# Optimization experiments

Hardware: AMD Instinct MI355X
Metric: run time of the kernel (lower is better)

Reference implementation:

```python
import jax, jax.numpy as jnp
import numpy as np

IN_CHANNELS = 512
NUM_HEADS = 8
PARTIAL = 4
PC = IN_CHANNELS // PARTIAL  # 128, per-branch dim


def _mha(x, wqkv, bqkv, wproj, bproj, num_heads):
    # Standard ViT-style attention block: fused qkv -> SDPA -> out proj.
    B, N, C = x.shape
    d = C // num_heads
    qkv = (x @ wqkv + bqkv).reshape(B, N, 3, num_heads, d)
    q, k, v = jnp.moveaxis(qkv, 2, 0)            # each (B, N, h, d)
    q = q.transpose(0, 2, 1, 3)                  # (B, h, N, d)
    k = k.transpose(0, 2, 1, 3)
    v = v.transpose(0, 2, 1, 3)
    scale = jnp.asarray(d, x.dtype) ** -0.5
    attn = jax.nn.softmax(jnp.einsum('bhqd,bhkd->bhqk', q, k) * scale, axis=-1)
    out = jnp.einsum('bhqk,bhkd->bhqd', attn, v)
    out = out.transpose(0, 2, 1, 3).reshape(B, N, C)
    return out @ wproj + bproj


def _channel_shuffle(x, groups):
    # ShuffleNet channel shuffle on (b, c, n, t)
    b, c, n, t = x.shape
    return x.reshape(b, groups, c // groups, n, t).transpose(0, 2, 1, 3, 4).reshape(b, c, n, t)


def setup_inputs() -> dict:
    key = jax.random.key(0)
    ks = jax.random.split(key, 13)
    b, n, t = 8, 25, 64
    inp = {'x': jax.random.normal(ks[0], (b, n, t, IN_CHANNELS), dtype=jnp.float32)}
    i = 1
    for name in ('t', 's', 'st'):
        inp[f'{name}_wqkv'] = jax.random.normal(ks[i], (PC, 3 * PC), dtype=jnp.float32) * 0.02; i += 1
        inp[f'{name}_bqkv'] = jnp.zeros((3 * PC,), dtype=jnp.float32)
        inp[f'{name}_wproj'] = jax.random.normal(ks[i], (PC, PC), dtype=jnp.float32) * 0.02; i += 1
        inp[f'{name}_bproj'] = jnp.zeros((PC,), dtype=jnp.float32)
    return inp


def reference(x, t_wqkv, t_bqkv, t_wproj, t_bproj,
              s_wqkv, s_bqkv, s_wproj, s_bproj,
              st_wqkv, st_bqkv, st_wproj, st_bproj):
    b, n, t, c = x.shape
    pc = PC
    # split order in forward: x_id, x_st, x_s, x_t (all width pc here)
    x_id = x[..., 0 * pc:1 * pc]
    x_st = x[..., 1 * pc:2 * pc]
    x_s = x[..., 2 * pc:3 * pc]
    x_t = x[..., 3 * pc:4 * pc]

    t_x = x_t.reshape(b * n, t, pc)                       # temporal: attend over t
    s_x = x_s.transpose(0, 2, 1, 3).reshape(b * t, n, pc)  # spatial: attend over n
    st_x = x_st.reshape(b, n * t, pc)                      # spatiotemporal: attend over n*t

    t_x = _mha(t_x, t_wqkv, t_bqkv, t_wproj, t_bproj, NUM_HEADS).reshape(b, n, t, pc)
    s_x = _mha(s_x, s_wqkv, s_bqkv, s_wproj, s_bproj, NUM_HEADS).reshape(b, t, n, pc).transpose(0, 2, 1, 3)
    st_x = _mha(st_x, st_wqkv, st_bqkv, st_wproj, st_bproj, NUM_HEADS).reshape(b, n, t, pc)

    # concat order: id, t, s, st (differs from split order), then to channels-first
    out = jnp.concatenate((x_id, t_x, s_x, st_x), axis=3).transpose(0, 3, 1, 2)  # (b, c, n, t)
    return _channel_shuffle(out, PARTIAL)
```

## Files before the change

### kernel.cpp

```cpp
#include <hip/hip_runtime.h>
#include <hip/hip_bf16.h>

#define BUF   1638400ull
#define QSC   0.36067376f

typedef __attribute__((ext_vector_type(4)))  float    f4;
typedef __attribute__((ext_vector_type(16))) float    f16v;
typedef __attribute__((ext_vector_type(8)))  short    s8v;
typedef __attribute__((ext_vector_type(4)))  unsigned u4v;

#if __has_builtin(__builtin_amdgcn_exp2f)
#define EXP2(x) __builtin_amdgcn_exp2f(x)
#else
#define EXP2(x) exp2f(x)
#endif
#if __has_builtin(__builtin_amdgcn_rcpf)
#define RCP(x) __builtin_amdgcn_rcpf(x)
#else
#define RCP(x) (1.0f/(x))
#endif

__device__ __forceinline__ short f2bf(float f) {
    __hip_bfloat16 h = __float2bfloat16(f);
    short s; __builtin_memcpy(&s, &h, 2); return s;
}
__device__ __forceinline__ unsigned pack2(float a, float b) {
    return (unsigned)(unsigned short)f2bf(a) | ((unsigned)(unsigned short)f2bf(b) << 16);
}
__device__ __forceinline__ float bf2f(short s) {
    return __uint_as_float((unsigned)(unsigned short)s << 16);
}
__device__ __forceinline__ unsigned tpack(float hi, float lo) {
    return __builtin_amdgcn_perm(__float_as_uint(hi), __float_as_uint(lo), 0x07060302u);
}
__device__ __forceinline__ f16v zf16() {
    f16v z;
#pragma unroll
    for (int i = 0; i < 16; i++) z[i] = 0.f;
    return z;
}

__global__ __launch_bounds__(256) void prep(
    const float* __restrict__ wq0, const float* __restrict__ wq1,
    const float* __restrict__ wq2,
    const float* __restrict__ wp0, const float* __restrict__ wp1,
    const float* __restrict__ wp2,
    short* __restrict__ wsw, short* __restrict__ onesb)
{
    const int blk = blockIdx.x, tid = threadIdx.x;
    if (blk < 96) {
        const int idx0 = blk * 2048 + tid * 8;
        const float* W; int Ncols, loc = idx0;
        if      (idx0 < 49152)  { W = wq0; Ncols = 384; }
        else if (idx0 < 98304)  { W = wq1; Ncols = 384; loc -= 49152; }
        else if (idx0 < 147456) { W = wq2; Ncols = 384; loc -= 98304; }
        else if (idx0 < 163840) { W = wp0; Ncols = 128; loc -= 147456; }
        else if (idx0 < 180224) { W = wp1; Ncols = 128; loc -= 163840; }
        else                    { W = wp2; Ncols = 128; loc -= 180224; }
        const int lane = (loc >> 3) & 63, ks = (loc >> 9) & 3, nt = loc >> 11;
        const int col = nt * 16 + (lane & 15);
        const int k0  = ks * 32 + 8 * (lane >> 4);
        s8v o;
#pragma unroll
        for (int j = 0; j < 8; j++) o[j] = f2bf(W[(k0 + j) * Ncols + col]);
        *(s8v*)(wsw + idx0) = o;
    } else {
        s8v o;
#pragma unroll
        for (int j = 0; j < 8; j++) o[j] = (short)0x3F80;
        *(s8v*)(onesb + tid * 8) = o;
    }
}

__global__ __launch_bounds__(256) void qkv_all(
    const float* __restrict__ x, const short* __restrict__ wsw,
    const float* __restrict__ bq0, const float* __restrict__ bq1,
    const float* __restrict__ bq2,
    short* __restrict__ q0, short* __restrict__ k0, short* __restrict__ vt0,
    short* __restrict__ q1, short* __restrict__ k1, short* __restrict__ vt1,
    short* __restrict__ q2, short* __restrict__ k2, short* __restrict__ vt2)
{
    const int br = blockIdx.x / 800, tile = blockIdx.x % 800;
    const int tok0 = tile * 16;
    const int wave = threadIdx.x >> 6, lane = threadIdx.x & 63;
    const int c = lane & 15, gq = lane >> 4;
    const int off = 384 - 128 * br;
    const short* wswb = wsw + br * 49152;
    const float* bias = (br == 0) ? bq0 : (br == 1) ? bq1 : bq2;

    const float* xrow = x + (size_t)(tok0 + c) * 512 + off + 8 * gq;
    s8v af[4];
#pragma unroll
    for (int ks = 0; ks < 4; ks++) {
        float4 a = *(const float4*)(xrow + ks * 32);
        float4 b = *(const float4*)(xrow + ks * 32 + 4);
        u4v t;
        t[0] = tpack(a.y, a.x); t[1] = tpack(a.w, a.z);
        t[2] = tpack(b.y, b.x); t[3] = tpack(b.w, b.z);
        af[ks] = __builtin_bit_cast(s8v, t);
    }

    const int batch0 = tok0 >> 6;
    const int b_  = tok0 / 1600;
    const int rm0 = tok0 - b_ * 1600;
    const int seq1 = rm0 >> 6;

    for (int nti = 0; nti < 6; nti++) {
        const int nt = wave * 6 + nti;
        const short* bp = wswb + ((size_t)(nt * 4) * 64 + lane) * 8;
        f4 acc = {0.f, 0.f, 0.f, 0.f};
#pragma unroll
        for (int ks = 0; ks < 4; ks++) {
            s8v bf = *(const s8v*)(bp + ks * 512);
            acc = __builtin_amdgcn_mfma_f32_16x16x32_bf16(af[ks], bf, acc, 0, 0, 0);
        }
        const float bv = bias[nt * 16 + c];
        const float v0 = acc[0]+bv, v1 = acc[1]+bv, v2 = acc[2]+bv, v3 = acc[3]+bv;
        const int which = nt >> 3, h = nt & 7;

        if (br == 0) {
            const int seq0 = (tok0 & 63) + 4 * gq;
            if (which == 2) {
                unsigned* p = (unsigned*)(vt0 + ((size_t)(batch0*8+h)*16 + c)*64 + seq0);
                p[0] = pack2(v0, v1); p[1] = pack2(v2, v3);
            } else {
                short* p = (which ? k0 : q0) + (((size_t)(batch0*8+h)*64 + seq0)*16 + c);
                p[0]=f2bf(v0); p[16]=f2bf(v1); p[32]=f2bf(v2); p[48]=f2bf(v3);
            }
        } else if (br == 1) {
            const int bt0 = b_ * 64 + (rm0 & 63) + 4 * gq;
            if (which == 2) {
                short* p = vt1 + ((size_t)(bt0*8+h)*16 + c)*32 + seq1;
                p[0]=f2bf(v0); p[4096]=f2bf(v1); p[8192]=f2bf(v2); p[12288]=f2bf(v3);
            } else {
                short* p = (which ? k1 : q1) + (((size_t)bt0*8+h)*25 + seq1)*16 + c;
                p[0]=f2bf(v0); p[3200]=f2bf(v1); p[6400]=f2bf(v2); p[9600]=f2bf(v3);
            }
        } else {
            const int seq0 = rm0 + 4 * gq;
            if (which == 2) {
                unsigned* p = (unsigned*)(vt2 + ((size_t)b_*128 + h*16 + c)*1600 + seq0);
                p[0] = pack2(v0, v1); p[1] = pack2(v2, v3);
            } else {
                short* p = (which ? k2 : q2) + (((size_t)b_*8+h)*1600 + seq0)*16 + c;
                p[0]=f2bf(v0); p[16]=f2bf(v1); p[32]=f2bf(v2); p[48]=f2bf(v3);
            }
        }
    }
}

template<int NSTEPS, bool MASK>
__device__ __forceinline__ void attn32(
    const short* __restrict__ qg, const short* __restrict__ kg,
    const short* __restrict__ vtg, const int vstride,
    const short* __restrict__ onesb,
    const int lane, const int qt0,
    short* __restrict__ obase, const int orowstride, const int nq)
{
    const int n = lane & 31, g2 = lane >> 5;

    s8v qraw = *(const s8v*)(qg + (size_t)(qt0 + n) * 16 + 8 * g2);
    u4v qu;
#pragma unroll
    for (int jp = 0; jp < 4; jp++)
        qu[jp] = tpack(bf2f(qraw[2*jp+1]) * QSC, bf2f(qraw[2*jp]) * QSC);
    const s8v qf = __builtin_bit_cast(s8v, qu);

    const int b4 = n >> 2;
    const int krow = ((b4 ^ (((b4 ^ (b4 >> 1)) & 1) * 3)) << 2) + (n & 3);
    const short* kp = kg + (size_t)krow * 16 + 8 * g2;
    const short* vp = (n < 16) ? (vtg + (size_t)n * vstride + 8 * g2)
                               : (onesb + 8 * g2);

    f16v oacc = zf16();

    for (int s = 0; s < NSTEPS; s++) {
        s8v kf  = *(const s8v*)kp;  kp += 512;
        s8v vf1 = *(const s8v*)vp;
        s8v vf2 = *(const s8v*)(vp + 16); vp += 32;

        f16v sacc = __builtin_amdgcn_mfma_f32_32x32x16_bf16(kf, qf, zf16(), 0, 0, 0);

        float p[16];
#pragma unroll
        for (int r = 0; r < 16; r++) {
            p[r] = EXP2(sacc[r]);
            if (MASK && r >= 9) { if (g2) p[r] = 0.f; }
        }
        u4v u1, u2;
        u1[0]=tpack(p[1],p[0]);   u1[1]=tpack(p[3],p[2]);
        u1[2]=tpack(p[5],p[4]);   u1[3]=tpack(p[7],p[6]);
        u2[0]=tpack(p[9],p[8]);   u2[1]=tpack(p[11],p[10]);
        u2[2]=tpack(p[13],p[12]); u2[3]=tpack(p[15],p[14]);
        s8v pf1 = __builtin_bit_cast(s8v, u1);
        s8v pf2 = __builtin_bit_cast(s8v, u2);

        oacc = __builtin_amdgcn_mfma_f32_32x32x16_bf16(pf1, vf1, oacc, 0, 0, 0);
        oacc = __builtin_amdgcn_mfma_f32_32x32x16_bf16(pf2, vf2, oacc, 0, 0, 0);
    }

#pragma unroll
    for (int r = 0; r < 16; r++) {
        float l = __shfl_xor(oacc[r], 16);
        float o = oacc[r] * RCP(l);
        const int q = qt0 + (r & 3) + 8 * (r >> 2) + 4 * g2;
        if (n < 16 && q < nq)
            obase[(size_t)q * orowstride + n] = f2bf(o);
    }
}

__global__ __launch_bounds__(256) void attn_all(
    const short* __restrict__ q0, const short* __restrict__ k0, const short* __restrict__ vt0,
    const short* __restrict__ q1, const short* __restrict__ k1, const short* __restrict__ vt1,
    const short* __restrict__ q2, const short* __restrict__ k2, const short* __restrict__ vt2,
    const short* __restrict__ onesb,
    short* __restrict__ ob0, short* __restrict__ ob1, short* __restrict__ ob2)
{
    const int wave = threadIdx.x >> 6, lane = threadIdx.x & 63;
    const int wid = blockIdx.x * 4 + wave;

    if (wid < 3200) {
        const int bh = wid / 50, qt0 = (wid % 50) * 32;
        const int batch = bh >> 3, h = bh & 7;
        attn32<50, false>(q2 + (size_t)bh * 25600, k2 + (size_t)bh * 25600,
                          vt2 + (size_t)batch * 204800 + (size_t)h * 16 * 1600, 1600,
                          onesb, lane, qt0,
                          ob2 + (size_t)batch * 204800 + h * 16, 128, 1600);
    } else if (wid < 6400) {
        const int w = wid - 3200;
        const int bh = w >> 1, qt0 = (w & 1) * 32;
        const int bn = bh >> 3, h = bh & 7;
        attn32<2, false>(q0 + (size_t)bh * 1024, k0 + (size_t)bh * 1024,
                         vt0 + (size_t)bh * 1024, 64,
                         onesb, lane, qt0,
                         ob0 + (size_t)bn * 8192 + h * 16, 128, 64);
    } else {
        const int bh = wid - 6400;
        if (bh < 4096) {
            const int bt = bh >> 3, h = bh & 7;
            const int b_ = bt >> 6, t_ = bt & 63;
            attn32<1, true>(q1 + (size_t)bh * 400, k1 + (size_t)bh * 400,
                            vt1 + (size_t)bh * 512, 32,
                            onesb, lane, 0,
                            ob1 + (size_t)b_ * 204800 + t_ * 128 + h * 16, 8192, 25);
        }
    }
}

__global__ __launch_bounds__(256) void projid(
    const short* __restrict__ ob0, const short* __restrict__ ob1,
    const short* __restrict__ ob2, const short* __restrict__ wsw,
    const float* __restrict__ bp0, const float* __restrict__ bp1,
    const float* __restrict__ bp2,
    const float* __restrict__ x, float* __restrict__ out)
{
    __shared__ unsigned short xl[64 * 130];
    const int blk = blockIdx.x, tid = threadIdx.x;

    if (blk < 2400) {
        const int br = blk / 800, t8 = blk % 800;
        const short* obb = (br == 0) ? ob0 : (br == 1) ? ob1 : ob2;
        const float* bp  = (br == 0) ? bp0 : (br == 1) ? bp1 : bp2;
        const short* wswb = wsw + 147456 + br * 16384;
        const int grp = br + 1;
        const int tok0 = t8 * 16;
        const int wave = tid >> 6, lane = tid & 63;
        const int c = lane & 15, gq = lane >> 4;

        s8v af[4];
#pragma unroll
        for (int ks = 0; ks < 4; ks++)
            af[ks] = *(const s8v*)(obb + (size_t)(tok0 + c) * 128 + ks * 32 + 8 * gq);

        const int bnn = t8 >> 2, b_ = bnn / 25, n_ = bnn % 25;
        const int t0 = (t8 & 3) * 16 + 4 * gq;

        for (int nti = 0; nti < 2; nti++) {
            const int nt = wave * 2 + nti;
            const short* bpw = wswb + ((size_t)(nt * 4) * 64 + lane) * 8;
            f4 acc = {0.f, 0.f, 0.f, 0.f};
#pragma unroll
            for (int ks = 0; ks < 4; ks++) {
                s8v bf = *(const s8v*)(bpw + ks * 512);
                acc = __builtin_amdgcn_mfma_f32_16x16x32_bf16(af[ks], bf, acc, 0, 0, 0);
            }
            const int c2 = nt * 16 + c;
            const float bv = bp[c2];
            float4 st = {acc[0]+bv, acc[1]+bv, acc[2]+bv, acc[3]+bv};
            *(float4*)(out + (size_t)b_ * 819200 + (size_t)(c2 * 4 + grp) * 1600
                           + n_ * 64 + t0) = st;
        }
    } else {
        const int bn = blk - 2400;
        const int b_ = bn / 25, n_ = bn % 25;
        for (int idx = tid; idx < 8192; idx += 256) {
            int row = idx >> 7, c2 = idx & 127;
            xl[row * 130 + c2] =
                (unsigned short)(__float_as_uint(x[(size_t)(bn * 64 + row) * 512 + c2]) >> 16);
        }
        __syncthreads();
        const int t_ = tid & 63, cg = tid >> 6;
        const size_t base = (size_t)b_ * 819200 + (size_t)n_ * 64 + t_;
#pragma unroll
        for (int i = 0; i < 32; i++) {
            int c2 = cg + 4 * i;
            out[base + (size_t)(c2 * 4 + 0) * 1600] =
                __uint_as_float((unsigned)xl[t_ * 130 + c2] << 16);
        }
    }
}

extern "C" void kernel_launch(void* const* d_in, const int* in_sizes, int n_in,
                              void* d_out, int out_size, void* d_ws, size_t ws_size,
                              hipStream_t stream)
{
    const float* x        = (const float*)d_in[0];
    const float* t_wqkv   = (const float*)d_in[1];
    const float* t_bqkv   = (const float*)d_in[2];
    const float* t_wproj  = (const float*)d_in[3];
    const float* t_bproj  = (const float*)d_in[4];
    const float* s_wqkv   = (const float*)d_in[5];
    const float* s_bqkv   = (const float*)d_in[6];
    const float* s_wproj  = (const float*)d_in[7];
    const float* s_bproj  = (const float*)d_in[8];
    const float* st_wqkv  = (const float*)d_in[9];
    const float* st_bqkv  = (const float*)d_in[10];
    const float* st_wproj = (const float*)d_in[11];
    const float* st_bproj = (const float*)d_in[12];

    short* wsw   = (short*)d_ws;
    short* onesb = wsw + 196608ull;
    short* q0  = onesb + 2048ull;
    short* k0  = q0 + BUF;
    short* vt0 = k0 + BUF;
    short* q1  = vt0 + BUF;
    short* k1  = q1 + BUF;
    short* vt1 = k1 + BUF;
    short* q2  = vt1 + 2097152ull;
    short* k2  = q2 + BUF;
    short* vt2 = k2 + BUF;
    short* ob0 = vt2 + BUF;
    short* ob1 = ob0 + BUF;
    short* ob2 = ob1 + BUF;
    float* out = (float*)d_out;

    prep<<<97, 256, 0, stream>>>(t_wqkv, s_wqkv, st_wqkv,
                                 t_wproj, s_wproj, st_wproj, wsw, onesb);
    qkv_all<<<2400, 256, 0, stream>>>(x, wsw, t_bqkv, s_bqkv, st_bqkv,
                                      q0, k0, vt0, q1, k1, vt1, q2, k2, vt2);
    attn_all<<<2624, 256, 0, stream>>>(q0, k0, vt0, q1, k1, vt1, q2, k2, vt2,
                                       onesb, ob0, ob1, ob2);
    projid<<<2600, 256, 0, stream>>>(ob0, ob1, ob2, wsw,
                                     t_bproj, s_bproj, st_bproj, x, out);
}
```

Measured before the change: 180.3 us.

## Split long spatiotemporal attention across four waves with shared-memory reduction

The n*t=1600-length attention branch previously ran as one wave per 32-query tile, looping over all 50 key tiles. Each such tile now gets its own block whose four waves each process a quarter of the key range. The partial (unnormalized) outputs and the row sums from the ones-column trick are added through LDS before normalization. This gives more parallelism and shorter serial chains for the long branch, at the cost of more blocks, LDS traffic, and a barrier. The grid grows accordingly. The approach is valid without a running max because scores are exponentiated directly, as in the code before.

Measured after the change: 174.8 us. 1.03x faster.

```diff
diff --git a/kernel.cpp b/kernel.cpp
--- a/kernel.cpp
+++ b/kernel.cpp
@@ -149,35 +149,38 @@
     }
 }
 
-template<int NSTEPS, bool MASK>
-__device__ __forceinline__ void attn32(
-    const short* __restrict__ qg, const short* __restrict__ kg,
-    const short* __restrict__ vtg, const int vstride,
-    const short* __restrict__ onesb,
-    const int lane, const int qt0,
-    short* __restrict__ obase, const int orowstride, const int nq)
+__device__ __forceinline__ s8v load_qfrag(const short* __restrict__ qg,
+                                          const int qt0, const int lane)
 {
     const int n = lane & 31, g2 = lane >> 5;
-
     s8v qraw = *(const s8v*)(qg + (size_t)(qt0 + n) * 16 + 8 * g2);
     u4v qu;
 #pragma unroll
     for (int jp = 0; jp < 4; jp++)
         qu[jp] = tpack(bf2f(qraw[2*jp+1]) * QSC, bf2f(qraw[2*jp]) * QSC);
-    const s8v qf = __builtin_bit_cast(s8v, qu);
-
+    return __builtin_bit_cast(s8v, qu);
+}
+
+template<bool MASK>
+__device__ __forceinline__ f16v attn_loop(
+    const short* __restrict__ kg, const short* __restrict__ vtg, const int vstride,
+    const short* __restrict__ onesb, const s8v qf, const int lane,
+    const int s0, const int s1)
+{
+    const int n = lane & 31, g2 = lane >> 5;
     const int b4 = n >> 2;
     const int krow = ((b4 ^ (((b4 ^ (b4 >> 1)) & 1) * 3)) << 2) + (n & 3);
-    const short* kp = kg + (size_t)krow * 16 + 8 * g2;
-    const short* vp = (n < 16) ? (vtg + (size_t)n * vstride + 8 * g2)
-                               : (onesb + 8 * g2);
+    const short* kp = kg + (size_t)(s0 * 32 + krow) * 16 + 8 * g2;
+    const short* vp;
+    int vinc;
+    if (n < 16) { vp = vtg + (size_t)n * vstride + s0 * 32 + 8 * g2; vinc = 32; }
+    else        { vp = onesb + 8 * g2; vinc = 0; }
 
     f16v oacc = zf16();
-
-    for (int s = 0; s < NSTEPS; s++) {
+    for (int s = s0; s < s1; s++) {
         s8v kf  = *(const s8v*)kp;  kp += 512;
         s8v vf1 = *(const s8v*)vp;
-        s8v vf2 = *(const s8v*)(vp + 16); vp += 32;
+        s8v vf2 = *(const s8v*)(vp + 16); vp += vinc;
 
         f16v sacc = __builtin_amdgcn_mfma_f32_32x32x16_bf16(kf, qf, zf16(), 0, 0, 0);
 
@@ -198,7 +201,14 @@
         oacc = __builtin_amdgcn_mfma_f32_32x32x16_bf16(pf1, vf1, oacc, 0, 0, 0);
         oacc = __builtin_amdgcn_mfma_f32_32x32x16_bf16(pf2, vf2, oacc, 0, 0, 0);
     }
-
+    return oacc;
+}
+
+__device__ __forceinline__ void attn_epilogue(
+    const f16v oacc, short* __restrict__ obase, const int orowstride,
+    const int qt0, const int nq, const int lane)
+{
+    const int n = lane & 31, g2 = lane >> 5;
 #pragma unroll
     for (int r = 0; r < 16; r++) {
         float l = __shfl_xor(oacc[r], 16);
@@ -216,34 +226,59 @@
     const short* __restrict__ onesb,
     short* __restrict__ ob0, short* __restrict__ ob1, short* __restrict__ ob2)
 {
+    __shared__ float red[4][64][16];
+    const int blk = blockIdx.x;
     const int wave = threadIdx.x >> 6, lane = threadIdx.x & 63;
-    const int wid = blockIdx.x * 4 + wave;
-
-    if (wid < 3200) {
-        const int bh = wid / 50, qt0 = (wid % 50) * 32;
+    const int n = lane & 31, g2 = lane >> 5;
+
+    if (blk < 3200) {
+        const int bh = blk / 50, qt0 = (blk % 50) * 32;
         const int batch = bh >> 3, h = bh & 7;
-        attn32<50, false>(q2 + (size_t)bh * 25600, k2 + (size_t)bh * 25600,
-                          vt2 + (size_t)batch * 204800 + (size_t)h * 16 * 1600, 1600,
-                          onesb, lane, qt0,
-                          ob2 + (size_t)batch * 204800 + h * 16, 128, 1600);
-    } else if (wid < 6400) {
-        const int w = wid - 3200;
-        const int bh = w >> 1, qt0 = (w & 1) * 32;
+        const s8v qf = load_qfrag(q2 + (size_t)bh * 25600, qt0, lane);
+        const int s0 = (50 * wave) >> 2, s1 = (50 * (wave + 1)) >> 2;
+        f16v part = attn_loop<false>(
+            k2 + (size_t)bh * 25600,
+            vt2 + (size_t)batch * 204800 + (size_t)h * 25600, 1600,
+            onesb, qf, lane, s0, s1);
+
+#pragma unroll
+        for (int j = 0; j < 4; j++) {
+            float4 v = {part[4*j], part[4*j+1], part[4*j+2], part[4*j+3]};
+            *(float4*)&red[wave][lane][4*j] = v;
+        }
+        __syncthreads();
+
+        short* obase = ob2 + (size_t)batch * 204800 + h * 16;
+#pragma unroll
+        for (int j = 0; j < 4; j++) {
+            const int r = 4 * wave + j;
+            float sum = red[0][lane][r] + red[1][lane][r]
+                      + red[2][lane][r] + red[3][lane][r];
+            float l = __shfl_xor(sum, 16);
+            float o = sum * RCP(l);
+            const int q = qt0 + (r & 3) + 8 * (r >> 2) + 4 * g2;
+            if (n < 16)
+                obase[(size_t)q * 128 + n] = f2bf(o);
+        }
+    } else if (blk < 4000) {
+        const int wid = (blk - 3200) * 4 + wave;
+        const int bh = wid >> 1, qt0 = (wid & 1) * 32;
         const int bn = bh >> 3, h = bh & 7;
-        attn32<2, false>(q0 + (size_t)bh * 1024, k0 + (size_t)bh * 1024,
-                         vt0 + (size_t)bh * 1024, 64,
-                         onesb, lane, qt0,
-                         ob0 + (size_t)bn * 8192 + h * 16, 128, 64);
+        const s8v qf = load_qfrag(q0 + (size_t)bh * 1024, qt0, lane);
+        f16v oacc = attn_loop<false>(k0 + (size_t)bh * 1024,
+                                     vt0 + (size_t)bh * 1024, 64,
+                                     onesb, qf, lane, 0, 2);
+        attn_epilogue(oacc, ob0 + (size_t)bn * 8192 + h * 16, 128, qt0, 64, lane);
     } else {
-        const int bh = wid - 6400;
-        if (bh < 4096) {
-            const int bt = bh >> 3, h = bh & 7;
-            const int b_ = bt >> 6, t_ = bt & 63;
-            attn32<1, true>(q1 + (size_t)bh * 400, k1 + (size_t)bh * 400,
-                            vt1 + (size_t)bh * 512, 32,
-                            onesb, lane, 0,
-                            ob1 + (size_t)b_ * 204800 + t_ * 128 + h * 16, 8192, 25);
-        }
+        const int bh = (blk - 4000) * 4 + wave;
+        const int bt = bh >> 3, h = bh & 7;
+        const int b_ = bt >> 6, t_ = bt & 63;
+        const s8v qf = load_qfrag(q1 + (size_t)bh * 400, 0, lane);
+        f16v oacc = attn_loop<true>(k1 + (size_t)bh * 400,
+                                    vt1 + (size_t)bh * 512, 32,
+                                    onesb, qf, lane, 0, 1);
+        attn_epilogue(oacc, ob1 + (size_t)b_ * 204800 + t_ * 128 + h * 16,
+                      8192, 0, 25, lane);
     }
 }
 
@@ -348,7 +383,7 @@
                                  t_wproj, s_wproj, st_wproj, wsw, onesb);
     qkv_all<<<2400, 256, 0, stream>>>(x, wsw, t_bqkv, s_bqkv, st_bqkv,
                                       q0, k0, vt0, q1, k1, vt1, q2, k2, vt2);
-    attn_all<<<2624, 256, 0, stream>>>(q0, k0, vt0, q1, k1, vt1, q2, k2, vt2,
+    attn_all<<<5024, 256, 0, stream>>>(q0, k0, vt0, q1, k1, vt1, q2, k2, vt2,
                                        onesb, ob0, ob1, ob2);
     projid<<<2600, 256, 0, stream>>>(ob0, ob1, ob2, wsw,
                                      t_bproj, s_bproj, st_bproj, x, out);
```
